# Performance work log

Hardware: AMD Instinct MI355X
Metric: run time of the kernel (lower is better)

The kernel has to match this reference:

```python
import jax, jax.numpy as jnp
import numpy as np

DIM = 256
HEADS = 8
DIM_HEAD = 32
SLICE_NUM = 64
B, N = 4, 32768


def setup_inputs() -> dict:
    key = jax.random.key(0)
    ks = jax.random.split(key, 8)
    inner = HEADS * DIM_HEAD
    s = 0.02
    x = jax.random.normal(ks[0], (B, N, DIM), dtype=jnp.float32)
    Wx = jax.random.normal(ks[1], (inner, DIM), dtype=jnp.float32) * s
    bx = jnp.zeros((inner,), dtype=jnp.float32)
    Wfx = jax.random.normal(ks[2], (inner, DIM), dtype=jnp.float32) * s
    bfx = jnp.zeros((inner,), dtype=jnp.float32)
    # orthogonal init for in_project_slice (S x D)
    g = jax.random.normal(ks[3], (SLICE_NUM, DIM_HEAD), dtype=jnp.float32)
    q, _ = jnp.linalg.qr(g.T)  # D x min(D,S); S>D so orthogonal columns
    Wslice = jnp.concatenate([q.T, jax.random.normal(ks[4], (SLICE_NUM - DIM_HEAD, DIM_HEAD)) * s], axis=0)
    bslice = jnp.zeros((SLICE_NUM,), dtype=jnp.float32)
    Wqkv = jax.random.normal(ks[5], (3 * DIM_HEAD, DIM_HEAD), dtype=jnp.float32) * s
    Wout = jax.random.normal(ks[6], (DIM, inner), dtype=jnp.float32) * s
    bout = jnp.zeros((DIM,), dtype=jnp.float32)
    temperature = jnp.ones((1, 1, HEADS, 1), dtype=jnp.float32) * 0.5
    return {"x": x, "Wx": Wx, "bx": bx, "Wfx": Wfx, "bfx": bfx,
            "Wslice": Wslice, "bslice": bslice, "Wqkv": Wqkv,
            "Wout": Wout, "bout": bout, "temperature": temperature}


def reference(x, Wx, bx, Wfx, bfx, Wslice, bslice, Wqkv, Wout, bout, temperature):
    b, n, c = x.shape
    inner = Wx.shape[0]
    d = Wqkv.shape[1]           # dim_head
    h = inner // d              # heads
    s = Wslice.shape[0]         # slice_num
    # project_input_onto_slices (irregular-mesh, standard Transolver)
    x_mid = (x @ Wx.T + bx).reshape(b, n, h, d)
    fx = (x @ Wfx.T + bfx).reshape(b, n, h, d)
    proj = jnp.einsum('bnhd,sd->bnhs', x_mid, Wslice) + bslice  # (B,N,H,S)
    # temperature-scaled softmax over slices
    temp = jnp.clip(temperature, 0.5, 5.0)  # (1,1,H,1)
    slice_weights = jax.nn.softmax(proj / temp, axis=-1)
    # pool tokens -> slice tokens
    slice_norm = slice_weights.sum(axis=1) + 0.01  # (B,H,S)
    normed = slice_weights / slice_norm[:, None, :, :]
    slice_token = jnp.einsum('bnhs,bnhd->bhsd', normed, fx)
    # small attention among slices (SDPA, scale = d^-0.5)
    qkv = jnp.einsum('bhsd,ed->bhse', slice_token, Wqkv)  # e = 3d
    q, k, v = jnp.split(qkv, 3, axis=-1)
    attn = jax.nn.softmax(jnp.einsum('bhqd,bhkd->bhqk', q, k) * (d ** -0.5), axis=-1)
    out_tok = jnp.einsum('bhqk,bhkd->bhqd', attn, v)  # (B,H,S,D)
    # unslice back to tokens
    out_x = jnp.einsum('bnhs,bhsd->bnhd', slice_weights, out_tok).reshape(b, n, inner)
    return out_x @ Wout.T + bout
```

## Files before the change

kernel.cpp:

```cpp
#include <hip/hip_runtime.h>

#define NB 4
#define NTOK 32768
#define BNT 131072
#define CDIM 256
#define HH 8
#define NCOL 768

typedef _Float16 f16;
typedef __attribute__((ext_vector_type(8))) _Float16 f16x8;
typedef __attribute__((ext_vector_type(4))) _Float16 f16x4;
typedef __attribute__((ext_vector_type(4))) float f32x4;

__device__ inline void gload_lds16(const void* g, void* l) {
    __builtin_amdgcn_global_load_lds(
        (const __attribute__((address_space(1))) void*)g,
        (__attribute__((address_space(3))) void*)l, 16, 0, 0);
}

__global__ __launch_bounds__(256) void xcvt(
    const float* __restrict__ x, f16* __restrict__ xf)
{
    long i = (long)blockIdx.x * 256 + threadIdx.x;
    const long stride = (long)gridDim.x * 256;
    const long n4 = (long)BNT * CDIM / 4;
    for (; i < n4; i += stride) {
        float4 v = ((const float4*)x)[i];
        f16x4 o = {(f16)v.x, (f16)v.y, (f16)v.z, (f16)v.w};
        *(f16x4*)(xf + i * 4) = o;
    }
}

__global__ __launch_bounds__(256) void k0_build(
    const float* __restrict__ Wx, const float* __restrict__ bx,
    const float* __restrict__ Wfx, const float* __restrict__ bfx,
    const float* __restrict__ Wslice, const float* __restrict__ bslice,
    f16* __restrict__ Bt, float* __restrict__ bcomb)
{
    int col = blockIdx.x;
    int k = threadIdx.x;
    float acc;
    if (col < 256) {
        acc = Wfx[col * 256 + k];
        if (k == 0) bcomb[col] = bfx[col];
    } else {
        int p = col - 256, h = p >> 6, s = p & 63;
        acc = 0.f;
        #pragma unroll
        for (int d = 0; d < 32; ++d)
            acc += Wx[(h * 32 + d) * 256 + k] * Wslice[s * 32 + d];
        if (k == 0) {
            float bacc = bslice[s];
            #pragma unroll
            for (int d = 0; d < 32; ++d)
                bacc += bx[h * 32 + d] * Wslice[s * 32 + d];
            bcomb[col] = bacc;
        }
    }
    Bt[(long)col * 256 + k] = (f16)acc;
}

template<int NSO, bool FUSE_SM>
__global__ __launch_bounds__(256) void gemm_f16(
    const f16* __restrict__ A, const f16* __restrict__ Bt,
    const float* __restrict__ bias, float* __restrict__ Cf,
    f16* __restrict__ Cfx, f16* __restrict__ Cw,
    const float* __restrict__ temperature, long bStrideB)
{
    constexpr int KO = NSO * 64;
    __shared__ char lds[65536];

    const int tid = threadIdx.x;
    const int lane = tid & 63;
    const int w = tid >> 6;
    const int wr = w >> 1, wc = w & 1;

    const int nx = gridDim.x;
    const int nwg = nx * gridDim.y;
    const int lid = blockIdx.y * nx + blockIdx.x;
    const int swz = (lid & 7) * (nwg >> 3) + (lid >> 3);
    const int m0 = (swz / nx) * 128, n0 = (swz % nx) * 128;

    const f16* BtB = Bt + ((long)m0 >> 15) * bStrideB;

    f32x4 acc[4][4] = {};

    auto stage = [&](int cs, int buf) {
        char* sa = lds + buf * 32768;
        char* sb = sa + 16384;
        #pragma unroll
        for (int i = 0; i < 4; ++i) {
            int li = i * 256 + tid;
            int r = li >> 3, c = li & 7;
            int csrc = c ^ (r & 7);
            int lb = (i * 256 + (tid & ~63)) * 16;
            long off = (long)cs * 64 + csrc * 8;
            gload_lds16(A + (long)(m0 + r) * KO + off, sa + lb);
            gload_lds16(BtB + (long)(n0 + r) * KO + off, sb + lb);
        }
    };

    stage(0, 0);
    __syncthreads();
    for (int cs = 0; cs < NSO; ++cs) {
        const int buf = cs & 1;
        if (cs + 1 < NSO) stage(cs + 1, buf ^ 1);
        const char* sa = lds + buf * 32768;
        const char* sb = sa + 16384;
        #pragma unroll
        for (int ksub = 0; ksub < 2; ++ksub) {
            int cr = ksub * 4 + (lane >> 4);
            f16x8 a[4], b[4];
            #pragma unroll
            for (int mi = 0; mi < 4; ++mi) {
                int r = wr * 64 + mi * 16 + (lane & 15);
                a[mi] = *(const f16x8*)(sa + r * 128 + ((cr ^ (r & 7)) << 4));
            }
            #pragma unroll
            for (int ni = 0; ni < 4; ++ni) {
                int r = wc * 64 + ni * 16 + (lane & 15);
                b[ni] = *(const f16x8*)(sb + r * 128 + ((cr ^ (r & 7)) << 4));
            }
            #pragma unroll
            for (int mi = 0; mi < 4; ++mi)
                #pragma unroll
                for (int ni = 0; ni < 4; ++ni)
                    acc[mi][ni] = __builtin_amdgcn_mfma_f32_16x16x32_f16(a[mi], b[ni], acc[mi][ni], 0, 0, 0);
        }
        __syncthreads();
    }
    {
        int rloc0 = wr * 64 + (lane >> 4) * 4;
        int cloc0 = wc * 64 + (lane & 15);
        float bv[4];
        #pragma unroll
        for (int ni = 0; ni < 4; ++ni) bv[ni] = bias[n0 + cloc0 + ni * 16];

        if constexpr (FUSE_SM) {
            f16* stile = (f16*)lds;
            bool proj = n0 >= 256;
            if (proj) {
                int h = (n0 - 256 + wc * 64) >> 6;
                float invt = 1.f / fminf(fmaxf(temperature[h], 0.5f), 5.0f);
                #pragma unroll
                for (int mi = 0; mi < 4; ++mi)
                    #pragma unroll
                    for (int rr = 0; rr < 4; ++rr) {
                        float v[4];
                        #pragma unroll
                        for (int ni = 0; ni < 4; ++ni)
                            v[ni] = (acc[mi][ni][rr] + bv[ni]) * invt;
                        float m = fmaxf(fmaxf(v[0], v[1]), fmaxf(v[2], v[3]));
                        #pragma unroll
                        for (int o = 1; o < 16; o <<= 1) m = fmaxf(m, __shfl_xor(m, o));
                        float e[4], s = 0.f;
                        #pragma unroll
                        for (int ni = 0; ni < 4; ++ni) { e[ni] = __expf(v[ni] - m); s += e[ni]; }
                        #pragma unroll
                        for (int o = 1; o < 16; o <<= 1) s += __shfl_xor(s, o);
                        float rs = 1.f / s;
                        int rloc = rloc0 + mi * 16 + rr;
                        #pragma unroll
                        for (int ni = 0; ni < 4; ++ni)
                            stile[rloc * 132 + cloc0 + ni * 16] = (f16)(e[ni] * rs);
                    }
            } else {
                #pragma unroll
                for (int mi = 0; mi < 4; ++mi)
                    #pragma unroll
                    for (int rr = 0; rr < 4; ++rr) {
                        int rloc = rloc0 + mi * 16 + rr;
                        #pragma unroll
                        for (int ni = 0; ni < 4; ++ni)
                            stile[rloc * 132 + cloc0 + ni * 16] =
                                (f16)(acc[mi][ni][rr] + bv[ni]);
                    }
            }
            __syncthreads();
            f16* dst = proj ? (Cw + (long)m0 * 512 + (n0 - 256))
                            : (Cfx + (long)m0 * 256 + n0);
            const int ld = proj ? 512 : 256;
            #pragma unroll
            for (int i = 0; i < 8; ++i) {
                int idx = i * 256 + tid;
                int r = idx >> 4, c = idx & 15;
                *(f16x8*)(dst + (long)r * ld + c * 8) =
                    *(const f16x8*)(stile + r * 132 + c * 8);
            }
        } else {
            #pragma unroll
            for (int mi = 0; mi < 4; ++mi)
                #pragma unroll
                for (int ni = 0; ni < 4; ++ni)
                    #pragma unroll
                    for (int rr = 0; rr < 4; ++rr)
                        Cf[(long)(m0 + rloc0 + mi * 16 + rr) * 256 + n0 + cloc0 + ni * 16] =
                            acc[mi][ni][rr] + bv[ni];
        }
    }
}

__global__ __launch_bounds__(256) void k1c_mfma(
    const f16* __restrict__ yfx, const f16* __restrict__ yw,
    float* __restrict__ partials)
{
    __shared__ char lds[49152];

    const int tid = threadIdx.x;
    const int lane = tid & 63;
    const int wv = tid >> 6;
    const int chunk64 = blockIdx.x & 63;
    const int bh = blockIdx.x >> 6;
    const int b = bh >> 3, h = bh & 7;
    const long tbase = (long)b * NTOK + (long)chunk64 * 512;

    f32x4 acc[4][3] = {};

    const f16 oe = ((lane & 15) == 0) ? (f16)1.0f : (f16)0.0f;
    const f16x8 bones = {oe, oe, oe, oe, oe, oe, oe, oe};
    const int g = lane >> 4;

    auto stage = [&](int iter, int buf) {
        const long t0 = tbase + iter * 128;
        char* base = lds + buf * 24576;
        #pragma unroll
        for (int i = 0; i < 4; ++i) {
            int k = wv * 4 + i;
            int sc = (lane & 7) ^ ((k & 3) << 1);
            gload_lds16(yw + (t0 + k * 8 + (lane >> 3)) * 512 + h * 64 + sc * 8,
                        base + k * 1024);
        }
        #pragma unroll
        for (int i = 0; i < 2; ++i) {
            int k = wv * 2 + i;
            int tq = (k & 1) * 16 + (lane >> 2);
            int dc = (lane & 3) ^ ((tq >> 3) & 3);
            gload_lds16(yfx + (t0 + k * 16 + (lane >> 2)) * 256 + h * 32 + dc * 8,
                        base + 16384 + k * 1024);
        }
    };

    stage(0, 0);
    for (int iter = 0; iter < 4; ++iter) {
        const int buf = iter & 1;
        if (iter < 3) {
            stage(iter + 1, buf ^ 1);
            asm volatile("s_waitcnt vmcnt(6)" ::: "memory");
        } else {
            asm volatile("s_waitcnt vmcnt(0)" ::: "memory");
        }
        __builtin_amdgcn_sched_barrier(0);
        const char* base = lds + buf * 24576;
        f16x8 a[4], bf[2];
        #pragma unroll
        for (int st = 0; st < 4; ++st) {
            int srow = st * 16 + (lane & 15);
            int schunk = (srow >> 3) ^ (g << 1);
            int off = wv * 4096 + g * 1024 + (schunk << 4) + (srow & 7) * 2;
            #pragma unroll
            for (int j = 0; j < 8; ++j)
                a[st][j] = *(const f16*)(base + off + j * 128);
        }
        #pragma unroll
        for (int dt = 0; dt < 2; ++dt) {
            int d = dt * 16 + (lane & 15);
            int dchunk = ((d >> 3) ^ g) & 3;
            int off = 16384 + wv * 2048 + g * 512 + (dchunk << 4) + (d & 7) * 2;
            #pragma unroll
            for (int j = 0; j < 8; ++j)
                bf[dt][j] = *(const f16*)(base + off + j * 64);
        }
        #pragma unroll
        for (int st = 0; st < 4; ++st) {
            acc[st][0] = __builtin_amdgcn_mfma_f32_16x16x32_f16(a[st], bf[0], acc[st][0], 0, 0, 0);
            acc[st][1] = __builtin_amdgcn_mfma_f32_16x16x32_f16(a[st], bf[1], acc[st][1], 0, 0, 0);
            acc[st][2] = __builtin_amdgcn_mfma_f32_16x16x32_f16(a[st], bones, acc[st][2], 0, 0, 0);
        }
    }
    __syncthreads();
    float* red = (float*)lds;
    #pragma unroll
    for (int st = 0; st < 4; ++st) {
        #pragma unroll
        for (int rr = 0; rr < 4; ++rr) {
            int s = st * 16 + g * 4 + rr;
            red[(wv * 64 + s) * 36 + (lane & 15)] = acc[st][0][rr];
            red[(wv * 64 + s) * 36 + 16 + (lane & 15)] = acc[st][1][rr];
            if ((lane & 15) == 0)
                red[(wv * 64 + s) * 36 + 32] = acc[st][2][rr];
        }
    }
    __syncthreads();
    float* P = partials + ((long)bh * 64 + chunk64) * 2112;
    for (int idx = tid; idx < 2112; idx += 256) {
        int s, c;
        if (idx < 2048) { s = idx >> 5; c = idx & 31; }
        else            { s = idx - 2048; c = 32; }
        float v = red[s * 36 + c] + red[(64 + s) * 36 + c]
                + red[(128 + s) * 36 + c] + red[(192 + s) * 36 + c];
        P[idx] = v;
    }
}

__global__ __launch_bounds__(256) void k3_slice(
    const float* __restrict__ partials,
    const float* __restrict__ Wqkv,
    const float* __restrict__ Wout,
    f16* __restrict__ OT2T)
{
    __shared__ float smem[14720];
    float* st = smem;
    float* q  = smem + 2112;
    float* kk = smem + 4224;
    float* v  = smem + 6336;
    float* L  = smem + 8448;
    float* red = L;
    float* ot = smem + 12608;

    int bh = blockIdx.x;
    int b = bh >> 3, h = bh & 7;
    int tid = threadIdx.x;

    for (int idx = tid; idx < 2112; idx += 256) {
        float s = 0.f;
        const float* P = partials + (long)bh * 64 * 2112 + idx;
        for (int c = 0; c < 64; ++c) s += P[c * 2112];
        red[idx] = s;
    }
    __syncthreads();
    for (int idx = tid; idx < 2048; idx += 256) {
        int s = idx >> 5, d = idx & 31;
        st[s * 33 + d] = red[idx] / (red[2048 + s] + 0.01f);
    }
    __syncthreads();
    for (int idx = tid; idx < 64 * 96; idx += 256) {
        int s = idx / 96, e = idx % 96;
        float acc = 0.f;
        #pragma unroll
        for (int d = 0; d < 32; ++d) acc += st[s * 33 + d] * Wqkv[e * 32 + d];
        if (e < 32)       q[s * 33 + e] = acc;
        else if (e < 64)  kk[s * 33 + (e - 32)] = acc;
        else              v[s * 33 + (e - 64)] = acc;
    }
    __syncthreads();
    for (int idx = tid; idx < 4096; idx += 256) {
        int i = idx >> 6, j = idx & 63;
        float acc = 0.f;
        #pragma unroll
        for (int d = 0; d < 32; ++d) acc += q[i * 33 + d] * kk[j * 33 + d];
        L[i * 65 + j] = acc * 0.17677669529663687f;
    }
    __syncthreads();
    {
        int lane = tid & 63, wid = tid >> 6;
        for (int r = wid; r < 64; r += 4) {
            float x = L[r * 65 + lane];
            float m = x;
            #pragma unroll
            for (int o = 32; o; o >>= 1) m = fmaxf(m, __shfl_xor(m, o));
            float e = __expf(x - m);
            float ss2 = e;
            #pragma unroll
            for (int o = 32; o; o >>= 1) ss2 += __shfl_xor(ss2, o);
            L[r * 65 + lane] = e / ss2;
        }
    }
    __syncthreads();
    for (int idx = tid; idx < 2048; idx += 256) {
        int s = idx >> 5, d = idx & 31;
        float acc = 0.f;
        #pragma unroll
        for (int j = 0; j < 64; ++j) acc += L[s * 65 + j] * v[j * 33 + d];
        ot[s * 33 + d] = acc;
    }
    __syncthreads();
    float* Wo = smem;
    for (int idx = tid; idx < 8192; idx += 256) {
        int c = idx >> 5, d = idx & 31;
        Wo[c * 33 + d] = Wout[c * 256 + h * 32 + d];
    }
    __syncthreads();
    {
        int c = tid;
        f16* O = OT2T + (long)b * 131072 + (long)c * 512 + h * 64;
        for (int s = 0; s < 64; ++s) {
            float acc = 0.f;
            #pragma unroll
            for (int d = 0; d < 32; ++d) acc += ot[s * 33 + d] * Wo[c * 33 + d];
            O[s] = (f16)acc;
        }
    }
}

extern "C" void kernel_launch(void* const* d_in, const int* in_sizes, int n_in,
                              void* d_out, int out_size, void* d_ws, size_t ws_size,
                              hipStream_t stream) {
    const float* x           = (const float*)d_in[0];
    const float* Wx          = (const float*)d_in[1];
    const float* bx          = (const float*)d_in[2];
    const float* Wfx         = (const float*)d_in[3];
    const float* bfx         = (const float*)d_in[4];
    const float* Wslice      = (const float*)d_in[5];
    const float* bslice      = (const float*)d_in[6];
    const float* Wqkv        = (const float*)d_in[7];
    const float* Wout        = (const float*)d_in[8];
    const float* bout        = (const float*)d_in[9];
    const float* temperature = (const float*)d_in[10];
    float* out = (float*)d_out;

    char* ws = (char*)d_ws;
    f16*   xf16     = (f16*)(ws);
    f16*   yfx      = (f16*)(ws + 67108864ULL);
    f16*   yw       = (f16*)(ws + 134217728ULL);
    float* partials = (float*)(ws + 268435456ULL);
    f16*   Bt       = (f16*)(ws + 285736960ULL);
    float* bcomb    = (float*)(ws + 286130176ULL);
    f16*   OT2T     = (f16*)(ws + 286133248ULL);

    k0_build<<<768, 256, 0, stream>>>(Wx, bx, Wfx, bfx, Wslice, bslice, Bt, bcomb);

    xcvt<<<2048, 256, 0, stream>>>(x, xf16);

    gemm_f16<4, true><<<dim3(NCOL / 128, BNT / 128), 256, 0, stream>>>(
        xf16, Bt, bcomb, nullptr, yfx, yw, temperature, 0L);

    k1c_mfma<<<32 * 64, 256, 0, stream>>>(yfx, yw, partials);

    k3_slice<<<32, 256, 0, stream>>>(partials, Wqkv, Wout, OT2T);

    gemm_f16<8, false><<<dim3(256 / 128, BNT / 128), 256, 0, stream>>>(
        yw, OT2T, bout, out, nullptr, nullptr, nullptr, 131072L);
}
```

Measured before the change: 375.4 us.

## Keep A row-panel resident in LDS and sweep all output columns per block

The first projection GEMM now has each block load its full 128x256 A row panel into LDS once and iterate over all six 128-column N tiles, double-buffering only the B tiles. This removes the six-fold re-reading of A across column-tile blocks. The epilogue now writes f16 results straight to global memory with strided scalar stores instead of staging through LDS for coalesced vector stores. It uses 128 KB of LDS per block, which limits occupancy to one block per CU, and the narrow stores may hurt write efficiency.

```diff
diff --git a/kernel.cpp b/kernel.cpp
--- a/kernel.cpp
+++ b/kernel.cpp
@@ -60,88 +60,99 @@
     Bt[(long)col * 256 + k] = (f16)acc;
 }
 
-template<int NSO, bool FUSE_SM>
-__global__ __launch_bounds__(256) void gemm_f16(
+__global__ __launch_bounds__(256) void k1a_big(
     const f16* __restrict__ A, const f16* __restrict__ Bt,
-    const float* __restrict__ bias, float* __restrict__ Cf,
-    f16* __restrict__ Cfx, f16* __restrict__ Cw,
-    const float* __restrict__ temperature, long bStrideB)
+    const float* __restrict__ bias, f16* __restrict__ Cfx,
+    f16* __restrict__ Cw, const float* __restrict__ temperature)
 {
-    constexpr int KO = NSO * 64;
-    __shared__ char lds[65536];
+    __shared__ char lds[131072];
 
     const int tid = threadIdx.x;
     const int lane = tid & 63;
     const int w = tid >> 6;
     const int wr = w >> 1, wc = w & 1;
-
-    const int nx = gridDim.x;
-    const int nwg = nx * gridDim.y;
-    const int lid = blockIdx.y * nx + blockIdx.x;
-    const int swz = (lid & 7) * (nwg >> 3) + (lid >> 3);
-    const int m0 = (swz / nx) * 128, n0 = (swz % nx) * 128;
-
-    const f16* BtB = Bt + ((long)m0 >> 15) * bStrideB;
-
-    f32x4 acc[4][4] = {};
-
-    auto stage = [&](int cs, int buf) {
-        char* sa = lds + buf * 32768;
-        char* sb = sa + 16384;
+    const int m0 = blockIdx.x * 128;
+
+    auto stageA = [&](int c) {
         #pragma unroll
         for (int i = 0; i < 4; ++i) {
             int li = i * 256 + tid;
-            int r = li >> 3, c = li & 7;
-            int csrc = c ^ (r & 7);
-            int lb = (i * 256 + (tid & ~63)) * 16;
-            long off = (long)cs * 64 + csrc * 8;
-            gload_lds16(A + (long)(m0 + r) * KO + off, sa + lb);
-            gload_lds16(BtB + (long)(n0 + r) * KO + off, sb + lb);
+            int r = li >> 3, cc = li & 7;
+            int csrc = cc ^ (r & 7);
+            gload_lds16(A + (long)(m0 + r) * 256 + c * 64 + csrc * 8,
+                        lds + c * 16384 + (i * 256 + (tid & ~63)) * 16);
         }
     };
-
-    stage(0, 0);
-    __syncthreads();
-    for (int cs = 0; cs < NSO; ++cs) {
-        const int buf = cs & 1;
-        if (cs + 1 < NSO) stage(cs + 1, buf ^ 1);
-        const char* sa = lds + buf * 32768;
-        const char* sb = sa + 16384;
-        #pragma unroll
-        for (int ksub = 0; ksub < 2; ++ksub) {
-            int cr = ksub * 4 + (lane >> 4);
-            f16x8 a[4], b[4];
-            #pragma unroll
-            for (int mi = 0; mi < 4; ++mi) {
-                int r = wr * 64 + mi * 16 + (lane & 15);
-                a[mi] = *(const f16x8*)(sa + r * 128 + ((cr ^ (r & 7)) << 4));
+    auto stageB = [&](int s, int buf) {
+        int j = s >> 1, h = s & 1;
+        #pragma unroll
+        for (int kc = 0; kc < 2; ++kc) {
+            #pragma unroll
+            for (int i = 0; i < 4; ++i) {
+                int li = i * 256 + tid;
+                int r = li >> 3, cc = li & 7;
+                int csrc = cc ^ (r & 7);
+                gload_lds16(Bt + (long)(j * 128 + r) * 256 + (h * 2 + kc) * 64 + csrc * 8,
+                            lds + 65536 + buf * 32768 + kc * 16384
+                                + (i * 256 + (tid & ~63)) * 16);
             }
-            #pragma unroll
-            for (int ni = 0; ni < 4; ++ni) {
-                int r = wc * 64 + ni * 16 + (lane & 15);
-                b[ni] = *(const f16x8*)(sb + r * 128 + ((cr ^ (r & 7)) << 4));
+        }
+    };
+
+    stageA(0); stageA(1); stageA(2); stageA(3);
+    stageB(0, 0);
+    __syncthreads();
+
+    f32x4 acc[4][4];
+
+    for (int s = 0; s < 12; ++s) {
+        const int j = s >> 1, h = s & 1;
+        const int buf = s & 1;
+        if (h == 0) {
+            #pragma unroll
+            for (int mi = 0; mi < 4; ++mi)
+                #pragma unroll
+                for (int ni = 0; ni < 4; ++ni)
+                    acc[mi][ni] = (f32x4){0.f, 0.f, 0.f, 0.f};
+        }
+        if (s + 1 < 12) stageB(s + 1, buf ^ 1);
+        const char* sb = lds + 65536 + buf * 32768;
+        #pragma unroll
+        for (int kc = 0; kc < 2; ++kc) {
+            const char* sa = lds + (h * 2 + kc) * 16384;
+            const char* sbk = sb + kc * 16384;
+            #pragma unroll
+            for (int ksub = 0; ksub < 2; ++ksub) {
+                int cr = ksub * 4 + (lane >> 4);
+                f16x8 a[4], b[4];
+                #pragma unroll
+                for (int mi = 0; mi < 4; ++mi) {
+                    int r = wr * 64 + mi * 16 + (lane & 15);
+                    a[mi] = *(const f16x8*)(sa + r * 128 + ((cr ^ (r & 7)) << 4));
+                }
+                #pragma unroll
+                for (int ni = 0; ni < 4; ++ni) {
+                    int r = wc * 64 + ni * 16 + (lane & 15);
+                    b[ni] = *(const f16x8*)(sbk + r * 128 + ((cr ^ (r & 7)) << 4));
+                }
+                #pragma unroll
+                for (int mi = 0; mi < 4; ++mi)
+                    #pragma unroll
+                    for (int ni = 0; ni < 4; ++ni)
+                        acc[mi][ni] = __builtin_amdgcn_mfma_f32_16x16x32_f16(
+                            a[mi], b[ni], acc[mi][ni], 0, 0, 0);
             }
-            #pragma unroll
-            for (int mi = 0; mi < 4; ++mi)
-                #pragma unroll
-                for (int ni = 0; ni < 4; ++ni)
-                    acc[mi][ni] = __builtin_amdgcn_mfma_f32_16x16x32_f16(a[mi], b[ni], acc[mi][ni], 0, 0, 0);
-        }
-        __syncthreads();
-    }
-    {
-        int rloc0 = wr * 64 + (lane >> 4) * 4;
-        int cloc0 = wc * 64 + (lane & 15);
-        float bv[4];
-        #pragma unroll
-        for (int ni = 0; ni < 4; ++ni) bv[ni] = bias[n0 + cloc0 + ni * 16];
-
-        if constexpr (FUSE_SM) {
-            f16* stile = (f16*)lds;
-            bool proj = n0 >= 256;
-            if (proj) {
-                int h = (n0 - 256 + wc * 64) >> 6;
-                float invt = 1.f / fminf(fmaxf(temperature[h], 0.5f), 5.0f);
+        }
+        if (h == 1) {
+            int rbase = m0 + wr * 64 + (lane >> 4) * 4;
+            int cbase = j * 128 + wc * 64 + (lane & 15);
+            float bv[4];
+            #pragma unroll
+            for (int ni = 0; ni < 4; ++ni) bv[ni] = bias[cbase + ni * 16];
+
+            if (j >= 2) {
+                int hh = (j * 128 + wc * 64 - 256) >> 6;
+                float invt = 1.f / fminf(fmaxf(temperature[hh], 0.5f), 5.0f);
                 #pragma unroll
                 for (int mi = 0; mi < 4; ++mi)
                     #pragma unroll
@@ -153,50 +164,115 @@
                         float m = fmaxf(fmaxf(v[0], v[1]), fmaxf(v[2], v[3]));
                         #pragma unroll
                         for (int o = 1; o < 16; o <<= 1) m = fmaxf(m, __shfl_xor(m, o));
-                        float e[4], s = 0.f;
+                        float e[4], ssum = 0.f;
                         #pragma unroll
-                        for (int ni = 0; ni < 4; ++ni) { e[ni] = __expf(v[ni] - m); s += e[ni]; }
+                        for (int ni = 0; ni < 4; ++ni) { e[ni] = __expf(v[ni] - m); ssum += e[ni]; }
                         #pragma unroll
-                        for (int o = 1; o < 16; o <<= 1) s += __shfl_xor(s, o);
-                        float rs = 1.f / s;
-                        int rloc = rloc0 + mi * 16 + rr;
+                        for (int o = 1; o < 16; o <<= 1) ssum += __shfl_xor(ssum, o);
+                        float rs = 1.f / ssum;
+                        long row = rbase + mi * 16 + rr;
                         #pragma unroll
                         for (int ni = 0; ni < 4; ++ni)
-                            stile[rloc * 132 + cloc0 + ni * 16] = (f16)(e[ni] * rs);
+                            Cw[row * 512 + cbase + ni * 16 - 256] = (f16)(e[ni] * rs);
                     }
             } else {
                 #pragma unroll
                 for (int mi = 0; mi < 4; ++mi)
                     #pragma unroll
                     for (int rr = 0; rr < 4; ++rr) {
-                        int rloc = rloc0 + mi * 16 + rr;
+                        long row = rbase + mi * 16 + rr;
                         #pragma unroll
                         for (int ni = 0; ni < 4; ++ni)
-                            stile[rloc * 132 + cloc0 + ni * 16] =
+                            Cfx[row * 256 + cbase + ni * 16] =
                                 (f16)(acc[mi][ni][rr] + bv[ni]);
                     }
             }
-            __syncthreads();
-            f16* dst = proj ? (Cw + (long)m0 * 512 + (n0 - 256))
-                            : (Cfx + (long)m0 * 256 + n0);
-            const int ld = proj ? 512 : 256;
-            #pragma unroll
-            for (int i = 0; i < 8; ++i) {
-                int idx = i * 256 + tid;
-                int r = idx >> 4, c = idx & 15;
-                *(f16x8*)(dst + (long)r * ld + c * 8) =
-                    *(const f16x8*)(stile + r * 132 + c * 8);
+        }
+        __syncthreads();
+    }
+}
+
+template<int NSO>
+__global__ __launch_bounds__(256) void gemm_f16(
+    const f16* __restrict__ A, const f16* __restrict__ Bt,
+    const float* __restrict__ bias, float* __restrict__ Cf, long bStrideB)
+{
+    constexpr int KO = NSO * 64;
+    __shared__ char lds[65536];
+
+    const int tid = threadIdx.x;
+    const int lane = tid & 63;
+    const int w = tid >> 6;
+    const int wr = w >> 1, wc = w & 1;
+
+    const int nx = gridDim.x;
+    const int nwg = nx * gridDim.y;
+    const int lid = blockIdx.y * nx + blockIdx.x;
+    const int swz = (lid & 7) * (nwg >> 3) + (lid >> 3);
+    const int m0 = (swz / nx) * 128, n0 = (swz % nx) * 128;
+
+    const f16* BtB = Bt + ((long)m0 >> 15) * bStrideB;
+
+    f32x4 acc[4][4] = {};
+
+    auto stage = [&](int cs, int buf) {
+        char* sa = lds + buf * 32768;
+        char* sb = sa + 16384;
+        #pragma unroll
+        for (int i = 0; i < 4; ++i) {
+            int li = i * 256 + tid;
+            int r = li >> 3, c = li & 7;
+            int csrc = c ^ (r & 7);
+            int lb = (i * 256 + (tid & ~63)) * 16;
+            long off = (long)cs * 64 + csrc * 8;
+            gload_lds16(A + (long)(m0 + r) * KO + off, sa + lb);
+            gload_lds16(BtB + (long)(n0 + r) * KO + off, sb + lb);
+        }
+    };
+
+    stage(0, 0);
+    __syncthreads();
+    for (int cs = 0; cs < NSO; ++cs) {
+        const int buf = cs & 1;
+        if (cs + 1 < NSO) stage(cs + 1, buf ^ 1);
+        const char* sa = lds + buf * 32768;
+        const char* sb = sa + 16384;
+        #pragma unroll
+        for (int ksub = 0; ksub < 2; ++ksub) {
+            int cr = ksub * 4 + (lane >> 4);
+            f16x8 a[4], b[4];
+            #pragma unroll
+            for (int mi = 0; mi < 4; ++mi) {
+                int r = wr * 64 + mi * 16 + (lane & 15);
+                a[mi] = *(const f16x8*)(sa + r * 128 + ((cr ^ (r & 7)) << 4));
             }
-        } else {
+            #pragma unroll
+            for (int ni = 0; ni < 4; ++ni) {
+                int r = wc * 64 + ni * 16 + (lane & 15);
+                b[ni] = *(const f16x8*)(sb + r * 128 + ((cr ^ (r & 7)) << 4));
+            }
             #pragma unroll
             for (int mi = 0; mi < 4; ++mi)
                 #pragma unroll
                 for (int ni = 0; ni < 4; ++ni)
-                    #pragma unroll
-                    for (int rr = 0; rr < 4; ++rr)
-                        Cf[(long)(m0 + rloc0 + mi * 16 + rr) * 256 + n0 + cloc0 + ni * 16] =
-                            acc[mi][ni][rr] + bv[ni];
-        }
+                    acc[mi][ni] = __builtin_amdgcn_mfma_f32_16x16x32_f16(a[mi], b[ni], acc[mi][ni], 0, 0, 0);
+        }
+        __syncthreads();
+    }
+    {
+        int rbase = m0 + wr * 64 + (lane >> 4) * 4;
+        int cbase = n0 + wc * 64 + (lane & 15);
+        float bv[4];
+        #pragma unroll
+        for (int ni = 0; ni < 4; ++ni) bv[ni] = bias[cbase + ni * 16];
+        #pragma unroll
+        for (int mi = 0; mi < 4; ++mi)
+            #pragma unroll
+            for (int ni = 0; ni < 4; ++ni)
+                #pragma unroll
+                for (int rr = 0; rr < 4; ++rr)
+                    Cf[(long)(rbase + mi * 16 + rr) * 256 + cbase + ni * 16] =
+                        acc[mi][ni][rr] + bv[ni];
     }
 }
 
@@ -421,13 +497,12 @@
 
     xcvt<<<2048, 256, 0, stream>>>(x, xf16);
 
-    gemm_f16<4, true><<<dim3(NCOL / 128, BNT / 128), 256, 0, stream>>>(
-        xf16, Bt, bcomb, nullptr, yfx, yw, temperature, 0L);
+    k1a_big<<<BNT / 128, 256, 0, stream>>>(xf16, Bt, bcomb, yfx, yw, temperature);
 
     k1c_mfma<<<32 * 64, 256, 0, stream>>>(yfx, yw, partials);
 
     k3_slice<<<32, 256, 0, stream>>>(partials, Wqkv, Wout, OT2T);
 
-    gemm_f16<8, false><<<dim3(256 / 128, BNT / 128), 256, 0, stream>>>(
-        yw, OT2T, bout, out, nullptr, nullptr, nullptr, 131072L);
-}
+    gemm_f16<8><<<dim3(256 / 128, BNT / 128), 256, 0, stream>>>(
+        yw, OT2T, bout, out, 131072L);
+}
```

Result: slower. 394.7 us (+5.1%).

## Widen GEMM tiles to 128x256 with 8 waves and triple-buffered K pipeline

Applied to the files above, without the earlier changes.

Replaces the 128x128, 4-wave GEMM with a 128x256, 8-wave kernel that uses K-steps of 32 and a three-stage LDS ring buffer. Global-to-LDS loads run two stages ahead, gated by explicit vmcnt waits and a single barrier per step. The LDS-staged coalesced epilogue is removed, so softmax and bias outputs are written straight to global memory as scattered f16 stores. Each A tile is now reused across more columns, but the stores are less coalesced and each wave gets fewer MFMAs per barrier.

```diff
diff --git a/kernel.cpp b/kernel.cpp
--- a/kernel.cpp
+++ b/kernel.cpp
@@ -61,86 +61,95 @@
 }
 
 template<int NSO, bool FUSE_SM>
-__global__ __launch_bounds__(256) void gemm_f16(
+__global__ __launch_bounds__(512) void gemm_w(
     const f16* __restrict__ A, const f16* __restrict__ Bt,
     const float* __restrict__ bias, float* __restrict__ Cf,
     f16* __restrict__ Cfx, f16* __restrict__ Cw,
     const float* __restrict__ temperature, long bStrideB)
 {
-    constexpr int KO = NSO * 64;
-    __shared__ char lds[65536];
+    constexpr int KO = NSO * 32;
+    __shared__ char lds[73728];
 
     const int tid = threadIdx.x;
     const int lane = tid & 63;
     const int w = tid >> 6;
-    const int wr = w >> 1, wc = w & 1;
+    const int wm = w >> 2, wn = w & 3;
 
     const int nx = gridDim.x;
     const int nwg = nx * gridDim.y;
     const int lid = blockIdx.y * nx + blockIdx.x;
     const int swz = (lid & 7) * (nwg >> 3) + (lid >> 3);
-    const int m0 = (swz / nx) * 128, n0 = (swz % nx) * 128;
+    const int m0 = (swz / nx) * 128, n0 = (swz % nx) * 256;
 
     const f16* BtB = Bt + ((long)m0 >> 15) * bStrideB;
 
     f32x4 acc[4][4] = {};
 
     auto stage = [&](int cs, int buf) {
-        char* sa = lds + buf * 32768;
-        char* sb = sa + 16384;
-        #pragma unroll
-        for (int i = 0; i < 4; ++i) {
-            int li = i * 256 + tid;
-            int r = li >> 3, c = li & 7;
-            int csrc = c ^ (r & 7);
-            int lb = (i * 256 + (tid & ~63)) * 16;
-            long off = (long)cs * 64 + csrc * 8;
-            gload_lds16(A + (long)(m0 + r) * KO + off, sa + lb);
-            gload_lds16(BtB + (long)(n0 + r) * KO + off, sb + lb);
+        char* base = lds + buf * 24576;
+        {
+            int r = tid >> 2, c = tid & 3;
+            int csrc = c ^ ((r >> 1) & 3);
+            gload_lds16(A + (long)(m0 + r) * KO + cs * 32 + csrc * 8,
+                        base + (tid & ~63) * 16);
+        }
+        #pragma unroll
+        for (int i = 0; i < 2; ++i) {
+            int q = (w * 2 + i) * 64 + lane;
+            int r = q >> 2, c = q & 3;
+            int csrc = c ^ ((r >> 1) & 3);
+            gload_lds16(BtB + (long)(n0 + r) * KO + cs * 32 + csrc * 8,
+                        base + 8192 + (w * 2 + i) * 1024);
         }
     };
 
     stage(0, 0);
-    __syncthreads();
+    stage(1, 1);
+    asm volatile("s_waitcnt vmcnt(3)" ::: "memory");
+    __builtin_amdgcn_sched_barrier(0);
+    __builtin_amdgcn_s_barrier();
+
     for (int cs = 0; cs < NSO; ++cs) {
-        const int buf = cs & 1;
-        if (cs + 1 < NSO) stage(cs + 1, buf ^ 1);
-        const char* sa = lds + buf * 32768;
-        const char* sb = sa + 16384;
-        #pragma unroll
-        for (int ksub = 0; ksub < 2; ++ksub) {
-            int cr = ksub * 4 + (lane >> 4);
-            f16x8 a[4], b[4];
-            #pragma unroll
-            for (int mi = 0; mi < 4; ++mi) {
-                int r = wr * 64 + mi * 16 + (lane & 15);
-                a[mi] = *(const f16x8*)(sa + r * 128 + ((cr ^ (r & 7)) << 4));
-            }
-            #pragma unroll
-            for (int ni = 0; ni < 4; ++ni) {
-                int r = wc * 64 + ni * 16 + (lane & 15);
-                b[ni] = *(const f16x8*)(sb + r * 128 + ((cr ^ (r & 7)) << 4));
-            }
-            #pragma unroll
-            for (int mi = 0; mi < 4; ++mi)
-                #pragma unroll
-                for (int ni = 0; ni < 4; ++ni)
-                    acc[mi][ni] = __builtin_amdgcn_mfma_f32_16x16x32_f16(a[mi], b[ni], acc[mi][ni], 0, 0, 0);
-        }
-        __syncthreads();
-    }
+        const int buf = cs % 3;
+        if (cs + 2 < NSO) stage(cs + 2, (cs + 2) % 3);
+        const char* sa = lds + buf * 24576;
+        const char* sb = sa + 8192;
+        const int cr = lane >> 4;
+        f16x8 a[4], b[4];
+        #pragma unroll
+        for (int mi = 0; mi < 4; ++mi) {
+            int r = wm * 64 + mi * 16 + (lane & 15);
+            a[mi] = *(const f16x8*)(sa + r * 64 + ((cr ^ ((r >> 1) & 3)) << 4));
+        }
+        #pragma unroll
+        for (int ni = 0; ni < 4; ++ni) {
+            int r = wn * 64 + ni * 16 + (lane & 15);
+            b[ni] = *(const f16x8*)(sb + r * 64 + ((cr ^ ((r >> 1) & 3)) << 4));
+        }
+        #pragma unroll
+        for (int mi = 0; mi < 4; ++mi)
+            #pragma unroll
+            for (int ni = 0; ni < 4; ++ni)
+                acc[mi][ni] = __builtin_amdgcn_mfma_f32_16x16x32_f16(
+                    a[mi], b[ni], acc[mi][ni], 0, 0, 0);
+        if (cs + 1 < NSO) {
+            if (cs + 2 < NSO) asm volatile("s_waitcnt vmcnt(3)" ::: "memory");
+            else              asm volatile("s_waitcnt vmcnt(0)" ::: "memory");
+            __builtin_amdgcn_sched_barrier(0);
+            __builtin_amdgcn_s_barrier();
+        }
+    }
+
     {
-        int rloc0 = wr * 64 + (lane >> 4) * 4;
-        int cloc0 = wc * 64 + (lane & 15);
+        int rbase = m0 + wm * 64 + (lane >> 4) * 4;
+        int cbase = n0 + wn * 64 + (lane & 15);
         float bv[4];
         #pragma unroll
-        for (int ni = 0; ni < 4; ++ni) bv[ni] = bias[n0 + cloc0 + ni * 16];
+        for (int ni = 0; ni < 4; ++ni) bv[ni] = bias[cbase + ni * 16];
 
         if constexpr (FUSE_SM) {
-            f16* stile = (f16*)lds;
-            bool proj = n0 >= 256;
-            if (proj) {
-                int h = (n0 - 256 + wc * 64) >> 6;
+            if (n0 > 0) {
+                int h = ((n0 - 256) >> 6) + wn;
                 float invt = 1.f / fminf(fmaxf(temperature[h], 0.5f), 5.0f);
                 #pragma unroll
                 for (int mi = 0; mi < 4; ++mi)
@@ -153,39 +162,28 @@
                         float m = fmaxf(fmaxf(v[0], v[1]), fmaxf(v[2], v[3]));
                         #pragma unroll
                         for (int o = 1; o < 16; o <<= 1) m = fmaxf(m, __shfl_xor(m, o));
-                        float e[4], s = 0.f;
-                        #pragma unroll
-                        for (int ni = 0; ni < 4; ++ni) { e[ni] = __expf(v[ni] - m); s += e[ni]; }
-                        #pragma unroll
-                        for (int o = 1; o < 16; o <<= 1) s += __shfl_xor(s, o);
-                        float rs = 1.f / s;
-                        int rloc = rloc0 + mi * 16 + rr;
+                        float e[4], ssum = 0.f;
+                        #pragma unroll
+                        for (int ni = 0; ni < 4; ++ni) { e[ni] = __expf(v[ni] - m); ssum += e[ni]; }
+                        #pragma unroll
+                        for (int o = 1; o < 16; o <<= 1) ssum += __shfl_xor(ssum, o);
+                        float rs = 1.f / ssum;
+                        long row = rbase + mi * 16 + rr;
                         #pragma unroll
                         for (int ni = 0; ni < 4; ++ni)
-                            stile[rloc * 132 + cloc0 + ni * 16] = (f16)(e[ni] * rs);
+                            Cw[row * 512 + cbase + ni * 16 - 256] = (f16)(e[ni] * rs);
                     }
             } else {
                 #pragma unroll
                 for (int mi = 0; mi < 4; ++mi)
                     #pragma unroll
                     for (int rr = 0; rr < 4; ++rr) {
-                        int rloc = rloc0 + mi * 16 + rr;
+                        long row = rbase + mi * 16 + rr;
                         #pragma unroll
                         for (int ni = 0; ni < 4; ++ni)
-                            stile[rloc * 132 + cloc0 + ni * 16] =
+                            Cfx[row * 256 + cbase + ni * 16] =
                                 (f16)(acc[mi][ni][rr] + bv[ni]);
                     }
-            }
-            __syncthreads();
-            f16* dst = proj ? (Cw + (long)m0 * 512 + (n0 - 256))
-                            : (Cfx + (long)m0 * 256 + n0);
-            const int ld = proj ? 512 : 256;
-            #pragma unroll
-            for (int i = 0; i < 8; ++i) {
-                int idx = i * 256 + tid;
-                int r = idx >> 4, c = idx & 15;
-                *(f16x8*)(dst + (long)r * ld + c * 8) =
-                    *(const f16x8*)(stile + r * 132 + c * 8);
             }
         } else {
             #pragma unroll
@@ -194,7 +192,7 @@
                 for (int ni = 0; ni < 4; ++ni)
                     #pragma unroll
                     for (int rr = 0; rr < 4; ++rr)
-                        Cf[(long)(m0 + rloc0 + mi * 16 + rr) * 256 + n0 + cloc0 + ni * 16] =
+                        Cf[(long)(rbase + mi * 16 + rr) * 256 + cbase + ni * 16] =
                             acc[mi][ni][rr] + bv[ni];
         }
     }
@@ -421,13 +419,13 @@
 
     xcvt<<<2048, 256, 0, stream>>>(x, xf16);
 
-    gemm_f16<4, true><<<dim3(NCOL / 128, BNT / 128), 256, 0, stream>>>(
+    gemm_w<8, true><<<dim3(NCOL / 256, BNT / 128), 512, 0, stream>>>(
         xf16, Bt, bcomb, nullptr, yfx, yw, temperature, 0L);
 
     k1c_mfma<<<32 * 64, 256, 0, stream>>>(yfx, yw, partials);
 
     k3_slice<<<32, 256, 0, stream>>>(partials, Wqkv, Wout, OT2T);
 
-    gemm_f16<8, false><<<dim3(256 / 128, BNT / 128), 256, 0, stream>>>(
+    gemm_w<16, false><<<dim3(1, BNT / 128), 512, 0, stream>>>(
         yw, OT2T, bout, out, nullptr, nullptr, nullptr, 131072L);
 }
```

Result: faster. 358.2 us (-4.6%).
